# Optimization experiments

Hardware: AMD Instinct MI355X
Metric: run time of the kernel (lower is better)

## Reference

```python
import jax, jax.numpy as jnp
import numpy as np

B, HH, WW, C, HEADS = 2, 128, 128, 256, 8
D = C // HEADS


def setup_inputs() -> dict:
    key = jax.random.key(0)
    ks = jax.random.split(key, 24)
    def nrm(k, shape, s=0.02):
        return jax.random.normal(k, shape, jnp.float32) * s
    inp = {
        'x_2': jax.random.normal(ks[0], (B, HH, WW, C), jnp.float32),
        'x_4': jax.random.normal(ks[1], (B, HH, WW, C), jnp.float32),
        'x_8': jax.random.normal(ks[2], (B, HH, WW, C), jnp.float32),
        'y':   jax.random.normal(ks[3], (B, HH, WW, C), jnp.float32),
        'Wqm': nrm(ks[4], (C, C)), 'Wkm': nrm(ks[5], (C, C)), 'Wvm': nrm(ks[6], (C, C)),
        'Wk2': nrm(ks[7], (C, C)), 'Wv2': nrm(ks[8], (C, C)),
        'Wk4': nrm(ks[9], (C, C)), 'Wv4': nrm(ks[10], (C, C)),
        'Wk8': nrm(ks[11], (C, C)), 'Wv8': nrm(ks[12], (C, C)),
        'rescalem': jnp.ones((HEADS, 1, 1), jnp.float32),
        'rescale2': jnp.ones((HEADS, 1, 1), jnp.float32),
        'rescale4': jnp.ones((HEADS, 1, 1), jnp.float32),
        'rescale8': jnp.ones((HEADS, 1, 1), jnp.float32),
        'Wproj': nrm(ks[13], (C, C)), 'bproj': jnp.zeros((C,), jnp.float32),
        'Wpos1': nrm(ks[14], (C, 1, 3, 3)), 'Wpos2': nrm(ks[15], (C, 1, 3, 3)),
    }
    return inp


def _l2norm(x):
    # F.normalize(p=2, dim=-1): x / max(||x||_2, eps)
    return x / jnp.maximum(jnp.linalg.norm(x, axis=-1, keepdims=True), 1e-12)


def _heads_T(t):
    # (b, n, h*d) -> (b, h, d, n)  (split heads then transpose last two dims)
    b, n, _ = t.shape
    return t.reshape(b, n, HEADS, D).transpose(0, 2, 3, 1)


def _dwconv(x, w):
    # x: NCHW, w: (C,1,3,3) depthwise
    return jax.lax.conv_general_dilated(
        x, w, (1, 1), 'SAME',
        dimension_numbers=('NCHW', 'OIHW', 'NCHW'),
        feature_group_count=C)


def reference(x_2, x_4, x_8, y,
              Wqm, Wkm, Wvm, Wk2, Wv2, Wk4, Wv4, Wk8, Wv8,
              rescalem, rescale2, rescale4, rescale8,
              Wproj, bproj, Wpos1, Wpos2):
    b, h, w, c = y.shape
    n = h * w
    x2 = x_2.reshape(b, n, c)
    x4 = x_4.reshape(b, n, c)
    x8 = x_8.reshape(b, n, c)
    yf = y.reshape(b, n, c)

    q_inpm = yf @ Wqm.T
    v_inpm = yf @ Wvm.T
    qm = _l2norm(_heads_T(q_inpm))  # (b,heads,d,n), L2-normalized over n

    def branch(k_inp, v_inp, rescale):
        k = _l2norm(_heads_T(k_inp))   # (b,heads,d,n)
        v = _heads_T(v_inp)            # (b,heads,d,n)
        attn = jnp.einsum('bhdn,bhen->bhde', k, qm) * rescale  # (b,heads,d,d)
        attn = jax.nn.softmax(attn, axis=-1)
        return jnp.einsum('bhde,bhen->bhdn', attn, v)

    # NOTE: original code uses rescale4 for the x8 branch (faithful to source).
    xo = (branch(yf @ Wkm.T, v_inpm, rescalem)
          + branch(x2 @ Wk2.T, x2 @ Wv2.T, rescale2)
          + branch(x4 @ Wk4.T, x4 @ Wv4.T, rescale4)
          + branch(x8 @ Wk8.T, x8 @ Wv8.T, rescale4))

    # (b,heads,d,n) -> (b,n,heads*d)
    xo = xo.transpose(0, 3, 1, 2).reshape(b, n, HEADS * D)
    out_c = (xo @ Wproj.T + bproj).reshape(b, h, w, c)

    p = v_inpm.reshape(b, h, w, c).transpose(0, 3, 1, 2)  # NCHW
    p = _dwconv(p, Wpos1)
    p = jax.nn.gelu(p, approximate=False)
    p = _dwconv(p, Wpos2)
    out_p = p.transpose(0, 2, 3, 1)

    return out_c + out_p
```

## Files before the change

### kernel.cpp

```cpp
#include <hip/hip_runtime.h>
#include <hip/hip_bf16.h>
#include <math.h>

typedef short bf16x8 __attribute__((ext_vector_type(8)));
typedef float f32x4 __attribute__((ext_vector_type(4)));

#define MFMA16(a,b,c) __builtin_amdgcn_mfma_f32_16x16x32_bf16(a,b,c,0,0,0)

__device__ inline short f2bf(float f){
  union{ __hip_bfloat16 h; short s; } u;
  u.h = __float2bfloat16(f);
  return u.s;
}
__device__ inline float bf2f(short s){
  uint32_t u = ((uint32_t)(uint16_t)s) << 16;
  return __builtin_bit_cast(float, u);
}
__device__ inline void store8bf(short* dst, float4 a, float4 b){
  union{ short s[8]; int4 q; } u;
  u.s[0]=f2bf(a.x); u.s[1]=f2bf(a.y); u.s[2]=f2bf(a.z); u.s[3]=f2bf(a.w);
  u.s[4]=f2bf(b.x); u.s[5]=f2bf(b.y); u.s[6]=f2bf(b.z); u.s[7]=f2bf(b.w);
  *(int4*)dst = u.q;
}

__device__ inline void gld16(const void* g, void* l){
  __builtin_amdgcn_global_load_lds(
      (const __attribute__((address_space(1))) unsigned int*)g,
      (__attribute__((address_space(3))) unsigned int*)l, 16, 0, 0);
}

#define BARC() do{ asm volatile("":::"memory"); __builtin_amdgcn_s_barrier(); \
                   asm volatile("":::"memory"); }while(0)

__global__ __launch_bounds__(256) void k_cvt(const float* __restrict__ src, short* __restrict__ dst, int n){
  int i = blockIdx.x*256 + threadIdx.x;
  if(i < n) dst[i] = f2bf(src[i]);
}

__global__ __launch_bounds__(256) void k_wvt(const float* __restrict__ wm, const float* __restrict__ w2,
                                             const float* __restrict__ w4, const float* __restrict__ w8,
                                             short* __restrict__ wvT){
  int t = blockIdx.x*256 + threadIdx.x;
  int br = t >> 16; int rem = t & 65535; int a = rem >> 8, j = rem & 255;
  const float* w = (br==0)? wm : (br==1)? w2 : (br==2)? w4 : w8;
  wvT[t] = f2bf(w[j*256 + a]);
}

__global__ __launch_bounds__(256) void k_wT(const float* __restrict__ w1, const float* __restrict__ w2,
                                            float* __restrict__ wT){
  int t = blockIdx.x*256 + threadIdx.x;
  if(t >= 4608) return;
  int cv = t / 2304; int rem = t % 2304; int tap = rem >> 8; int c = rem & 255;
  const float* w = cv ? w2 : w1;
  wT[t] = w[c*9 + tap];
}

__global__ __launch_bounds__(256) void k_pack(const float* __restrict__ x2, const float* __restrict__ x4,
                                              const float* __restrict__ x8, const float* __restrict__ y,
                                              short* __restrict__ xt){
  int sb = blockIdx.z; int s = sb >> 1, b = sb & 1;
  const float* src = ((s==0)? y : (s==1)? x2 : (s==2)? x4 : x8) + (size_t)b*16384*256;
  __shared__ short tile[64*264];
  int t = threadIdx.x, l = t & 63, w = t >> 6;
  int n0 = blockIdx.x*64;
  #pragma unroll
  for(int p=0;p<16;++p){
    int row = p*4 + w;
    float4 v = *(const float4*)(src + (size_t)(n0+row)*256 + 4*l);
    union{ short s4[4]; int2 q; } u;
    u.s4[0]=f2bf(v.x); u.s4[1]=f2bf(v.y); u.s4[2]=f2bf(v.z); u.s4[3]=f2bf(v.w);
    *(int2*)&tile[row*264 + 4*l] = u.q;
  }
  __syncthreads();
  int c = t;
  short* outb = xt + ((size_t)sb*512 + (n0>>5))*8192;
  int sw = (c>>1)&3;
  #pragma unroll
  for(int ti=0; ti<2; ++ti){
    union{ short v[32]; int4 q4[4]; } rowv;
    #pragma unroll
    for(int j=0;j<32;++j) rowv.v[j] = tile[(ti*32+j)*264 + c];
    char* ob = (char*)(outb + (size_t)ti*8192 + c*32);
    #pragma unroll
    for(int hi=0;hi<4;++hi)
      *(int4*)(ob + ((hi ^ sw)<<4)) = rowv.q4[hi];
  }
}

__device__ inline bf16x8 tfrag(const short* base, int c, int hi){
  int byte = c*64 + ((hi ^ ((c>>1)&3))<<4);
  return *(const bf16x8*)((const char*)base + byte);
}

__global__ __launch_bounds__(512,2) void k_cov(const short* __restrict__ xt, float* __restrict__ covF){
  int jb = blockIdx.x;
  int ck = blockIdx.y;
  int j = jb >> 1, b = jb & 1;
  int t = threadIdx.x, l = t & 63, w = t >> 6;
  int lr = l & 15, hi = l >> 4;
  __shared__ short lds2[2][16384];
  int su = (j < 4) ? 0 : (j - 3);
  int sv = (j == 0) ? 0 : ((j < 4) ? j : (j - 3));
  int sym = (su == sv);
  const short* Ug = xt + (size_t)(su*2+b)*512*8192;
  const short* Vg = xt + (size_t)(sv*2+b)*512*8192;
  int nt0 = ck*32;

  f32x4 acc[2][16];
  #pragma unroll
  for(int i=0;i<2;++i)
    #pragma unroll
    for(int n2=0;n2<16;++n2) acc[i][n2] = (f32x4){0.f,0.f,0.f,0.f};

  #define STAGE_S(bufi, kk) do{                                                 \
    const short* Ut_ = Ug + (size_t)(nt0+(kk))*8192;                            \
    short* dst_ = &lds2[bufi][0];                                               \
    _Pragma("unroll")                                                           \
    for(int i_=0;i_<2;++i_){ int ch_ = w*2+i_;                                  \
      gld16(Ut_ + ch_*512 + l*8, dst_ + ch_*512); }                             \
  }while(0)
  #define STAGE_A(bufi, kk) do{                                                 \
    const short* Ut_ = Ug + (size_t)(nt0+(kk))*8192;                            \
    const short* Vt_ = Vg + (size_t)(nt0+(kk))*8192;                            \
    short* dst_ = &lds2[bufi][0];                                               \
    _Pragma("unroll")                                                           \
    for(int i_=0;i_<4;++i_){ int ch_ = w*4+i_;                                  \
      const short* g_ = (ch_<16) ? (Ut_ + ch_*512 + l*8)                        \
                                 : (Vt_ + (ch_-16)*512 + l*8);                  \
      gld16(g_, dst_ + ch_*512); }                                              \
  }while(0)

  #define COMPUTE(cur, vofs) do{                                                \
    const short* Ub_ = &lds2[cur][0];                                           \
    const short* Vb_ = Ub_ + (vofs);                                            \
    bf16x8 a0_ = tfrag(Ub_, w*32 + lr, hi);                                     \
    bf16x8 a1_ = tfrag(Ub_, w*32 + 16 + lr, hi);                                \
    _Pragma("unroll")                                                           \
    for(int nt_=0;nt_<16;++nt_){                                                \
      bf16x8 bb_ = tfrag(Vb_, nt_*16 + lr, hi);                                 \
      acc[0][nt_] = MFMA16(a0_, bb_, acc[0][nt_]);                              \
      acc[1][nt_] = MFMA16(a1_, bb_, acc[1][nt_]);                              \
    }                                                                           \
  }while(0)

  if(sym){
    STAGE_S(0, 0);
    STAGE_S(1, 1);
    asm volatile("s_waitcnt vmcnt(2)":::"memory");
    BARC();
    for(int k=0;k<32;++k){
      int cur = k & 1;
      COMPUTE(cur, 0);
      if(k == 31) break;
      BARC();
      if(k+2 < 32){
        STAGE_S(cur, k+2);
        asm volatile("s_waitcnt vmcnt(2)":::"memory");
      } else {
        asm volatile("s_waitcnt vmcnt(0)":::"memory");
      }
      BARC();
    }
  } else {
    STAGE_A(0, 0);
    STAGE_A(1, 1);
    asm volatile("s_waitcnt vmcnt(4)":::"memory");
    BARC();
    for(int k=0;k<32;++k){
      int cur = k & 1;
      COMPUTE(cur, 8192);
      if(k == 31) break;
      BARC();
      if(k+2 < 32){
        STAGE_A(cur, k+2);
        asm volatile("s_waitcnt vmcnt(4)":::"memory");
      } else {
        asm volatile("s_waitcnt vmcnt(0)":::"memory");
      }
      BARC();
    }
  }
  #undef STAGE_S
  #undef STAGE_A
  #undef COMPUTE

  float* cov = covF + (size_t)jb*65536;
  #pragma unroll
  for(int rt=0;rt<2;++rt)
    #pragma unroll
    for(int nt=0;nt<16;++nt)
      #pragma unroll
      for(int r=0;r<4;++r){
        int row = w*32 + rt*16 + 4*hi + r;
        int col = nt*16 + lr;
        atomicAdd(&cov[(size_t)row*256 + col], acc[rt][nt][r]);
      }
}

__device__ inline void mm_32x256(const short (*wA)[264], const short* __restrict__ covbf,
                                 short (*tmp)[264], int t){
  int l = t & 63, w = t >> 6;
  int mt = w >> 1, ntb = (w & 1)*8;
  f32x4 acc[8];
  #pragma unroll
  for(int i=0;i<8;++i) acc[i] = (f32x4){0.f,0.f,0.f,0.f};
  #pragma unroll
  for(int kk=0; kk<8; ++kk){
    bf16x8 a = *(const bf16x8*)&wA[16*mt + (l&15)][kk*32 + 8*(l>>4)];
    #pragma unroll
    for(int n=0; n<8; ++n){
      int j = (ntb+n)*16 + (l&15);
      bf16x8 bb = *(const bf16x8*)&covbf[(size_t)j*256 + kk*32 + 8*(l>>4)];
      acc[n] = MFMA16(a, bb, acc[n]);
    }
  }
  #pragma unroll
  for(int n=0;n<8;++n)
    #pragma unroll
    for(int r=0;r<4;++r)
      tmp[16*mt + 4*(l>>4) + r][(ntb+n)*16 + (l&15)] = f2bf(acc[n][r]);
}
__device__ inline void mm_32x32(const short (*A)[264], const short (*Bw)[264], float (*M)[33], int t){
  int l = t & 63, w = t >> 6;
  int mt = w >> 1, nt = w & 1;
  f32x4 acc = (f32x4){0.f,0.f,0.f,0.f};
  #pragma unroll
  for(int kk=0; kk<8; ++kk){
    bf16x8 a = *(const bf16x8*)&A[16*mt + (l&15)][kk*32 + 8*(l>>4)];
    bf16x8 b = *(const bf16x8*)&Bw[16*nt + (l&15)][kk*32 + 8*(l>>4)];
    acc = MFMA16(a, b, acc);
  }
  #pragma unroll
  for(int r=0;r<4;++r)
    M[16*mt + 4*(l>>4) + r][16*nt + (l&15)] = acc[r];
}

__global__ __launch_bounds__(256) void k_attn(
    const float* __restrict__ Wq, const float* __restrict__ Wkm, const float* __restrict__ Wk2,
    const float* __restrict__ Wk4, const float* __restrict__ Wk8,
    const float* __restrict__ rsm, const float* __restrict__ rs2, const float* __restrict__ rs4,
    const short* __restrict__ covB, float* __restrict__ Aout){
  int h = blockIdx.x, b = blockIdx.y, br = blockIdx.z;
  int t = threadIdx.x;
  __shared__ short wk[32][264], wq[32][264], tmp[32][264];
  __shared__ float Ml[32][33];
  __shared__ float nrm[64];
  const float* Wk = (br==0)? Wkm : (br==1)? Wk2 : (br==2)? Wk4 : Wk8;
  {
    int d = t >> 3, c0 = (t & 7)*32;
    const float* pk = Wk + (size_t)(h*32+d)*256 + c0;
    const float* pq = Wq + (size_t)(h*32+d)*256 + c0;
    #pragma unroll
    for(int i=0;i<32;i+=8){
      float4 a1 = *(const float4*)(pk+i), a2 = *(const float4*)(pk+i+4);
      store8bf(&wk[d][c0+i], a1, a2);
      float4 b1 = *(const float4*)(pq+i), b2 = *(const float4*)(pq+i+4);
      store8bf(&wq[d][c0+i], b1, b2);
    }
  }
  __syncthreads();
  const short* cxy = covB + (size_t)(br*2+b)*65536;
  const short* cxx = (br==0)? cxy : covB + (size_t)(8 + (br-1)*2 + b)*65536;
  const short* cyy = covB + (size_t)b*65536;
  mm_32x256(wk, cxx, tmp, t); __syncthreads();
  mm_32x32(tmp, wk, Ml, t);   __syncthreads();
  if(t < 32) nrm[t] = Ml[t][t];
  __syncthreads();
  mm_32x256(wq, cyy, tmp, t); __syncthreads();
  mm_32x32(tmp, wq, Ml, t);   __syncthreads();
  if(t < 32) nrm[32+t] = Ml[t][t];
  __syncthreads();
  mm_32x256(wk, cxy, tmp, t); __syncthreads();
  mm_32x32(tmp, wq, Ml, t);   __syncthreads();
  if(t < 32){
    int d = t;
    const float* rs = (br==0)? rsm : (br==1)? rs2 : rs4;
    float rsv = rs[h];
    float invk = 1.f / fmaxf(sqrtf(fmaxf(nrm[d], 0.f)), 1e-12f);
    float lg[32]; float mx = -1e30f;
    #pragma unroll
    for(int e=0;e<32;++e){
      float invq = 1.f / fmaxf(sqrtf(fmaxf(nrm[32+e], 0.f)), 1e-12f);
      float v = Ml[d][e] * invk * invq * rsv;
      lg[e] = v; mx = fmaxf(mx, v);
    }
    float sum = 0.f;
    #pragma unroll
    for(int e=0;e<32;++e){ lg[e] = expf(lg[e]-mx); sum += lg[e]; }
    float inv = 1.f/sum;
    float* Ao = Aout + ((size_t)((br*2+b)*8 + h))*1024 + d*32;
    #pragma unroll
    for(int e=0;e<32;++e) Ao[e] = lg[e]*inv;
  }
}

__global__ __launch_bounds__(256) void k_qfold(const float* __restrict__ Wproj, const float* __restrict__ Ain,
                                               const short* __restrict__ wvT, short* __restrict__ qf){
  int cg = blockIdx.x, b = blockIdx.y, br = blockIdx.z;
  int t = threadIdx.x;
  __shared__ float Al[8*1036];
  __shared__ short pl[32][264];
  const float* Ag = Ain + (size_t)((br*2+b)*8)*1024;
  for(int i=t; i<8192; i+=256){
    int hh = i >> 10, dd = (i >> 5) & 31, ee = i & 31;
    Al[hh*1036 + dd*32 + ee] = Ag[i];
  }
  __syncthreads();
  {
    int c = cg*32 + (t >> 3), h = t & 7;
    const float* wpr = Wproj + (size_t)c*256 + h*32;
    float wp[32];
    #pragma unroll
    for(int i=0;i<32;i+=4){
      float4 v = *(const float4*)(wpr+i);
      wp[i]=v.x; wp[i+1]=v.y; wp[i+2]=v.z; wp[i+3]=v.w;
    }
    float pv[32];
    #pragma unroll
    for(int e=0;e<32;++e) pv[e]=0.f;
    const float* Ah = Al + h*1036;
    #pragma unroll
    for(int d=0; d<32; ++d){
      float wpd = wp[d];
      #pragma unroll
      for(int e=0;e<32;e+=4){
        float4 av = *(const float4*)&Ah[d*32+e];
        pv[e]   += wpd*av.x; pv[e+1] += wpd*av.y;
        pv[e+2] += wpd*av.z; pv[e+3] += wpd*av.w;
      }
    }
    #pragma unroll
    for(int e=0;e<32;++e) pl[t>>3][h*32+e] = f2bf(pv[e]);
  }
  __syncthreads();
  {
    int l = t & 63, w = t >> 6, mt = w >> 1, ntb = (w & 1)*8;
    const short* wvt = wvT + (size_t)br*65536;
    f32x4 acc[8];
    #pragma unroll
    for(int i=0;i<8;++i) acc[i] = (f32x4){0.f,0.f,0.f,0.f};
    #pragma unroll
    for(int kk=0; kk<8; ++kk){
      bf16x8 a = *(const bf16x8*)&pl[16*mt + (l&15)][kk*32 + 8*(l>>4)];
      #pragma unroll
      for(int n=0;n<8;++n){
        int arow = (ntb+n)*16 + (l&15);
        bf16x8 bb = *(const bf16x8*)&wvt[(size_t)arow*256 + kk*32 + 8*(l>>4)];
        acc[n] = MFMA16(a, bb, acc[n]);
      }
    }
    short* qfp = qf + (size_t)(br*2+b)*65536;
    #pragma unroll
    for(int n=0;n<8;++n)
      #pragma unroll
      for(int r=0;r<4;++r){
        int row = cg*32 + 16*mt + 4*(l>>4) + r;
        int col = (ntb+n)*16 + (l&15);
        qfp[(size_t)row*256 + col] = f2bf(acc[n][r]);
      }
  }
}

__device__ inline void at_write4(short* base, int row, int l, float4 v){
  union{ short s[4]; int2 q; } u;
  u.s[0]=f2bf(v.x); u.s[1]=f2bf(v.y); u.s[2]=f2bf(v.z); u.s[3]=f2bf(v.w);
  int byte = row*512 + 8*l;
  byte ^= ((row&7)<<4);
  *(int2*)((char*)base + byte) = u.q;
}
__device__ inline bf16x8 at_read8(const short* base, int row, int kk, int q){
  int byte = row*512 + kk*64 + q*16;
  byte ^= ((row&7)<<4);
  return *(const bf16x8*)((const char*)base + byte);
}

__global__ __launch_bounds__(256,2) void k_vm(const float* __restrict__ y, const short* __restrict__ wB,
                                              short* __restrict__ vm){
  int t = threadIdx.x, l = t & 63, w = t >> 6;
  size_t m0 = (size_t)blockIdx.x*64;
  __shared__ short at[64*256];
  #pragma unroll
  for(int rr=0; rr<16; ++rr){
    int row = w*16 + rr;
    float4 v = *(const float4*)(y + (m0+row)*256 + 4*l);
    at_write4(at, row, l, v);
  }
  __syncthreads();
  f32x4 acc[4][4];
  #pragma unroll
  for(int i=0;i<4;++i)
    #pragma unroll
    for(int n2=0;n2<4;++n2) acc[i][n2] = (f32x4){0.f,0.f,0.f,0.f};
  #pragma unroll
  for(int kk=0; kk<8; ++kk){
    bf16x8 a[4];
    #pragma unroll
    for(int rt=0;rt<4;++rt) a[rt] = at_read8(at, rt*16 + (l&15), kk, l>>4);
    #pragma unroll
    for(int nt=0;nt<4;++nt){
      int bc = (w*4+nt)*16 + (l&15);
      bf16x8 bb = *(const bf16x8*)&wB[(size_t)bc*256 + kk*32 + 8*(l>>4)];
      #pragma unroll
      for(int rt=0;rt<4;++rt) acc[rt][nt] = MFMA16(a[rt], bb, acc[rt][nt]);
    }
  }
  #pragma unroll
  for(int rt=0;rt<4;++rt)
    #pragma unroll
    for(int nt=0;nt<4;++nt)
      #pragma unroll
      for(int r=0;r<4;++r){
        size_t row = m0 + rt*16 + 4*(l>>4) + r;
        int col = (w*4+nt)*16 + (l&15);
        vm[row*256 + col] = f2bf(acc[rt][nt][r]);
      }
}

__global__ __launch_bounds__(256) void k_conv(const short* __restrict__ in, const float* __restrict__ wT,
                                              short* __restrict__ out, int do_gelu){
  int tid = blockIdx.x*256 + threadIdx.x;
  int cg = tid & 31; int pix = tid >> 5;
  int x = pix & 127, yy = (pix >> 7) & 127, b = pix >> 14;
  int c0 = cg*8;
  float acc[8];
  #pragma unroll
  for(int i=0;i<8;++i) acc[i]=0.f;
  #pragma unroll
  for(int ky=0; ky<3; ++ky){
    int sy = yy + ky - 1;
    if(sy < 0 || sy > 127) continue;
    #pragma unroll
    for(int kx=0; kx<3; ++kx){
      int sx = x + kx - 1;
      if(sx < 0 || sx > 127) continue;
      const float* wp = wT + (ky*3+kx)*256 + c0;
      float4 w0 = *(const float4*)wp;
      float4 w1 = *(const float4*)(wp+4);
      const short* p = in + ((size_t)(((b<<7)+sy)<<7) + sx)*256 + c0;
      union{ int4 q; short s[8]; } u;
      u.q = *(const int4*)p;
      acc[0] += bf2f(u.s[0])*w0.x; acc[1] += bf2f(u.s[1])*w0.y;
      acc[2] += bf2f(u.s[2])*w0.z; acc[3] += bf2f(u.s[3])*w0.w;
      acc[4] += bf2f(u.s[4])*w1.x; acc[5] += bf2f(u.s[5])*w1.y;
      acc[6] += bf2f(u.s[6])*w1.z; acc[7] += bf2f(u.s[7])*w1.w;
    }
  }
  if(do_gelu){
    #pragma unroll
    for(int cc=0;cc<8;++cc)
      acc[cc] = 0.5f*acc[cc]*(1.f + erff(acc[cc]*0.70710678118654752f));
  }
  union{ int4 q; short s[8]; } o;
  #pragma unroll
  for(int cc=0;cc<8;++cc) o.s[cc] = f2bf(acc[cc]);
  *(int4*)(out + (size_t)pix*256 + c0) = o.q;
}

__global__ __launch_bounds__(256,2) void k_final(const float* __restrict__ y, const float* __restrict__ x2,
                                                 const float* __restrict__ x4, const float* __restrict__ x8,
                                                 const short* __restrict__ qf, const float* __restrict__ bproj,
                                                 const short* __restrict__ pos, float* __restrict__ out){
  int t = threadIdx.x, l = t & 63, w = t >> 6;
  size_t m0 = (size_t)blockIdx.x*64;
  int b = (int)(m0 >> 14);
  __shared__ short at[64*256];
  f32x4 acc[4][4];
  #pragma unroll
  for(int i=0;i<4;++i)
    #pragma unroll
    for(int n2=0;n2<4;++n2) acc[i][n2] = (f32x4){0.f,0.f,0.f,0.f};
  const float* srcs[4] = {y, x2, x4, x8};
  #pragma unroll 1
  for(int br=0; br<4; ++br){
    __syncthreads();
    #pragma unroll
    for(int rr=0; rr<16; ++rr){
      int row = w*16 + rr;
      float4 v = *(const float4*)(srcs[br] + (m0+row)*256 + 4*l);
      at_write4(at, row, l, v);
    }
    __syncthreads();
    const short* qb = qf + (size_t)(br*2+b)*65536;
    #pragma unroll
    for(int kk=0; kk<8; ++kk){
      bf16x8 a[4];
      #pragma unroll
      for(int rt=0;rt<4;++rt) a[rt] = at_read8(at, rt*16 + (l&15), kk, l>>4);
      #pragma unroll
      for(int nt=0;nt<4;++nt){
        int bc = (w*4+nt)*16 + (l&15);
        bf16x8 bb = *(const bf16x8*)&qb[(size_t)bc*256 + kk*32 + 8*(l>>4)];
        #pragma unroll
        for(int rt=0;rt<4;++rt) acc[rt][nt] = MFMA16(a[rt], bb, acc[rt][nt]);
      }
    }
  }
  #pragma unroll
  for(int rt=0;rt<4;++rt)
    #pragma unroll
    for(int nt=0;nt<4;++nt)
      #pragma unroll
      for(int r=0;r<4;++r){
        size_t row = m0 + rt*16 + 4*(l>>4) + r;
        int col = (w*4+nt)*16 + (l&15);
        out[row*256 + col] = acc[rt][nt][r] + bproj[col] + bf2f(pos[row*256 + col]);
      }
}

extern "C" void kernel_launch(void* const* d_in, const int* in_sizes, int n_in,
                              void* d_out, int out_size, void* d_ws, size_t ws_size,
                              hipStream_t stream){
  (void)in_sizes; (void)n_in; (void)out_size; (void)ws_size;
  const float* x2   = (const float*)d_in[0];
  const float* x4   = (const float*)d_in[1];
  const float* x8   = (const float*)d_in[2];
  const float* y    = (const float*)d_in[3];
  const float* Wq   = (const float*)d_in[4];
  const float* Wkm  = (const float*)d_in[5];
  const float* Wvm  = (const float*)d_in[6];
  const float* Wk2  = (const float*)d_in[7];
  const float* Wv2  = (const float*)d_in[8];
  const float* Wk4  = (const float*)d_in[9];
  const float* Wv4  = (const float*)d_in[10];
  const float* Wk8  = (const float*)d_in[11];
  const float* Wv8  = (const float*)d_in[12];
  const float* rsm  = (const float*)d_in[13];
  const float* rs2  = (const float*)d_in[14];
  const float* rs4  = (const float*)d_in[15];
  const float* Wproj= (const float*)d_in[17];
  const float* bproj= (const float*)d_in[18];
  const float* Wp1  = (const float*)d_in[19];
  const float* Wp2  = (const float*)d_in[20];
  float* out = (float*)d_out;

  char* ws = (char*)d_ws;
  short* XT2  = (short*)(ws + 0);
  short* VM   = (short*)(ws + 0);
  short* GBUF = (short*)(ws + 16777216);
  short* POS  = (short*)(ws + 33554432);
  float* wT   = (float*)(ws + 50331648);
  float* covF = (float*)(ws + 67108864);
  short* covB = (short*)(ws + 70778880);
  float* Aout = (float*)(ws + 72613888);
  short* QF   = (short*)(ws + 72876032);
  short* WvmB = (short*)(ws + 73924608);
  short* WvT  = (short*)(ws + 74055680);

  hipMemsetAsync(covF, 0, 3670016, stream);
  k_cvt  <<<256, 256, 0, stream>>>(Wvm, WvmB, 65536);
  k_wvt  <<<1024, 256, 0, stream>>>(Wvm, Wv2, Wv4, Wv8, WvT);
  k_pack <<<dim3(256,1,8), 256, 0, stream>>>(x2, x4, x8, y, XT2);
  k_cov  <<<dim3(14,16), 512, 0, stream>>>(XT2, covF);
  k_cvt  <<<3584, 256, 0, stream>>>(covF, covB, 917504);
  k_wT   <<<18, 256, 0, stream>>>(Wp1, Wp2, wT);
  k_attn <<<dim3(8,2,4), 256, 0, stream>>>(Wq, Wkm, Wk2, Wk4, Wk8, rsm, rs2, rs4, covB, Aout);
  k_qfold<<<dim3(8,2,4), 256, 0, stream>>>(Wproj, Aout, WvT, QF);
  k_vm   <<<512, 256, 0, stream>>>(y, WvmB, VM);
  k_conv <<<4096, 256, 0, stream>>>(VM, wT, GBUF, 1);
  k_conv <<<4096, 256, 0, stream>>>(GBUF, wT + 2304, POS, 0);
  k_final<<<512, 256, 0, stream>>>(y, x2, x4, x8, QF, bproj, POS, out);
}
```

Measured before the change: 288.2 us.

## Reuse bf16 row-major inputs, triple-buffer covariance, split atomic accumulation copies

k_pack now also writes a row-major bf16 copy of all four inputs. The V projection and final kernels read that copy instead of re-reading and converting the fp32 inputs. The covariance kernel moves from double to triple LDS buffering and spreads its accumulation across four copies indexed by chunk, which a new conversion kernel sums. This path runs only when the workspace is large enough, and it costs extra workspace, more LDS per block, and a larger memset.

```diff
diff --git a/kernel.cpp b/kernel.cpp
--- a/kernel.cpp
+++ b/kernel.cpp
@@ -35,6 +35,15 @@
 __global__ __launch_bounds__(256) void k_cvt(const float* __restrict__ src, short* __restrict__ dst, int n){
   int i = blockIdx.x*256 + threadIdx.x;
   if(i < n) dst[i] = f2bf(src[i]);
+}
+
+__global__ __launch_bounds__(256) void k_cvtN(const float* __restrict__ src, short* __restrict__ dst,
+                                              int n, int ncpy){
+  int i = blockIdx.x*256 + threadIdx.x;
+  if(i >= n) return;
+  float s = src[i];
+  for(int c=1;c<ncpy;++c) s += src[i + (size_t)c*917504];
+  dst[i] = f2bf(s);
 }
 
 __global__ __launch_bounds__(256) void k_wvt(const float* __restrict__ wm, const float* __restrict__ w2,
@@ -57,7 +66,7 @@
 
 __global__ __launch_bounds__(256) void k_pack(const float* __restrict__ x2, const float* __restrict__ x4,
                                               const float* __restrict__ x8, const float* __restrict__ y,
-                                              short* __restrict__ xt){
+                                              short* __restrict__ xt, short* __restrict__ xb){
   int sb = blockIdx.z; int s = sb >> 1, b = sb & 1;
   const float* src = ((s==0)? y : (s==1)? x2 : (s==2)? x4 : x8) + (size_t)b*16384*256;
   __shared__ short tile[64*264];
@@ -70,6 +79,7 @@
     union{ short s4[4]; int2 q; } u;
     u.s4[0]=f2bf(v.x); u.s4[1]=f2bf(v.y); u.s4[2]=f2bf(v.z); u.s4[3]=f2bf(v.w);
     *(int2*)&tile[row*264 + 4*l] = u.q;
+    if(xb) *(int2*)(xb + ((size_t)sb*16384 + n0 + row)*256 + 4*l) = u.q;
   }
   __syncthreads();
   int c = t;
@@ -92,13 +102,14 @@
   return *(const bf16x8*)((const char*)base + byte);
 }
 
-__global__ __launch_bounds__(512,2) void k_cov(const short* __restrict__ xt, float* __restrict__ covF){
+__global__ __launch_bounds__(512,2) void k_cov(const short* __restrict__ xt, float* __restrict__ covF,
+                                               int ncpy){
   int jb = blockIdx.x;
   int ck = blockIdx.y;
   int j = jb >> 1, b = jb & 1;
   int t = threadIdx.x, l = t & 63, w = t >> 6;
   int lr = l & 15, hi = l >> 4;
-  __shared__ short lds2[2][16384];
+  __shared__ short lds3[3][16384];
   int su = (j < 4) ? 0 : (j - 3);
   int sv = (j == 0) ? 0 : ((j < 4) ? j : (j - 3));
   int sym = (su == sv);
@@ -114,7 +125,7 @@
 
   #define STAGE_S(bufi, kk) do{                                                 \
     const short* Ut_ = Ug + (size_t)(nt0+(kk))*8192;                            \
-    short* dst_ = &lds2[bufi][0];                                               \
+    short* dst_ = &lds3[bufi][0];                                               \
     _Pragma("unroll")                                                           \
     for(int i_=0;i_<2;++i_){ int ch_ = w*2+i_;                                  \
       gld16(Ut_ + ch_*512 + l*8, dst_ + ch_*512); }                             \
@@ -122,16 +133,15 @@
   #define STAGE_A(bufi, kk) do{                                                 \
     const short* Ut_ = Ug + (size_t)(nt0+(kk))*8192;                            \
     const short* Vt_ = Vg + (size_t)(nt0+(kk))*8192;                            \
-    short* dst_ = &lds2[bufi][0];                                               \
+    short* dst_ = &lds3[bufi][0];                                               \
     _Pragma("unroll")                                                           \
     for(int i_=0;i_<4;++i_){ int ch_ = w*4+i_;                                  \
       const short* g_ = (ch_<16) ? (Ut_ + ch_*512 + l*8)                        \
                                  : (Vt_ + (ch_-16)*512 + l*8);                  \
       gld16(g_, dst_ + ch_*512); }                                              \
   }while(0)
-
-  #define COMPUTE(cur, vofs) do{                                                \
-    const short* Ub_ = &lds2[cur][0];                                           \
+  #define COMPUTE(bufp, vofs) do{                                               \
+    const short* Ub_ = bufp;                                                    \
     const short* Vb_ = Ub_ + (vofs);                                            \
     bf16x8 a0_ = tfrag(Ub_, w*32 + lr, hi);                                     \
     bf16x8 a1_ = tfrag(Ub_, w*32 + 16 + lr, hi);                                \
@@ -144,47 +154,53 @@
   }while(0)
 
   if(sym){
-    STAGE_S(0, 0);
-    STAGE_S(1, 1);
-    asm volatile("s_waitcnt vmcnt(2)":::"memory");
+    STAGE_S(0,0); STAGE_S(1,1); STAGE_S(2,2);
+    asm volatile("s_waitcnt vmcnt(4)":::"memory");
     BARC();
+    int buf = 0;
+    #pragma unroll 1
     for(int k=0;k<32;++k){
-      int cur = k & 1;
-      COMPUTE(cur, 0);
-      if(k == 31) break;
+      COMPUTE(&lds3[buf][0], 0);
+      if(k==31) break;
       BARC();
-      if(k+2 < 32){
-        STAGE_S(cur, k+2);
+      if(k < 29){
+        STAGE_S(buf, k+3);
+        asm volatile("s_waitcnt vmcnt(4)":::"memory");
+      } else if(k == 29){
         asm volatile("s_waitcnt vmcnt(2)":::"memory");
       } else {
         asm volatile("s_waitcnt vmcnt(0)":::"memory");
       }
       BARC();
+      buf = (buf==2)?0:(buf+1);
     }
   } else {
-    STAGE_A(0, 0);
-    STAGE_A(1, 1);
-    asm volatile("s_waitcnt vmcnt(4)":::"memory");
+    STAGE_A(0,0); STAGE_A(1,1); STAGE_A(2,2);
+    asm volatile("s_waitcnt vmcnt(8)":::"memory");
     BARC();
+    int buf = 0;
+    #pragma unroll 1
     for(int k=0;k<32;++k){
-      int cur = k & 1;
-      COMPUTE(cur, 8192);
-      if(k == 31) break;
+      COMPUTE(&lds3[buf][0], 8192);
+      if(k==31) break;
       BARC();
-      if(k+2 < 32){
-        STAGE_A(cur, k+2);
+      if(k < 29){
+        STAGE_A(buf, k+3);
+        asm volatile("s_waitcnt vmcnt(8)":::"memory");
+      } else if(k == 29){
         asm volatile("s_waitcnt vmcnt(4)":::"memory");
       } else {
         asm volatile("s_waitcnt vmcnt(0)":::"memory");
       }
       BARC();
+      buf = (buf==2)?0:(buf+1);
     }
   }
   #undef STAGE_S
   #undef STAGE_A
   #undef COMPUTE
 
-  float* cov = covF + (size_t)jb*65536;
+  float* cov = covF + (size_t)(ck & (ncpy-1))*917504 + (size_t)jb*65536;
   #pragma unroll
   for(int rt=0;rt<2;++rt)
     #pragma unroll
@@ -416,6 +432,42 @@
       }
 }
 
+__global__ __launch_bounds__(256) void k_vm_g(const short* __restrict__ xb, const short* __restrict__ wB,
+                                              short* __restrict__ vm){
+  int t = threadIdx.x, l = t & 63, w = t >> 6;
+  size_t m0 = (size_t)blockIdx.x*64;
+  int lr = l & 15, hq = (l >> 4)*8;
+  f32x4 acc[4][4];
+  #pragma unroll
+  for(int i=0;i<4;++i)
+    #pragma unroll
+    for(int n2=0;n2<4;++n2) acc[i][n2] = (f32x4){0.f,0.f,0.f,0.f};
+  #pragma unroll
+  for(int kk=0; kk<8; ++kk){
+    int k = kk*32 + hq;
+    bf16x8 a[4];
+    #pragma unroll
+    for(int rt=0;rt<4;++rt)
+      a[rt] = *(const bf16x8*)(xb + (m0 + rt*16 + lr)*256 + k);
+    #pragma unroll
+    for(int nt=0;nt<4;++nt){
+      bf16x8 bb = *(const bf16x8*)(wB + (size_t)((w*4+nt)*16 + lr)*256 + k);
+      #pragma unroll
+      for(int rt=0;rt<4;++rt) acc[rt][nt] = MFMA16(a[rt], bb, acc[rt][nt]);
+    }
+  }
+  #pragma unroll
+  for(int rt=0;rt<4;++rt)
+    #pragma unroll
+    for(int nt=0;nt<4;++nt)
+      #pragma unroll
+      for(int r=0;r<4;++r){
+        size_t row = m0 + rt*16 + 4*(l>>4) + r;
+        int col = (w*4+nt)*16 + lr;
+        vm[row*256 + col] = f2bf(acc[rt][nt][r]);
+      }
+}
+
 __global__ __launch_bounds__(256) void k_conv(const short* __restrict__ in, const float* __restrict__ wT,
                                               short* __restrict__ out, int do_gelu){
   int tid = blockIdx.x*256 + threadIdx.x;
@@ -507,10 +559,53 @@
       }
 }
 
+__global__ __launch_bounds__(256) void k_final_g(const short* __restrict__ xb, const short* __restrict__ qf,
+                                                 const float* __restrict__ bproj, const short* __restrict__ pos,
+                                                 float* __restrict__ out){
+  int t = threadIdx.x, l = t & 63, w = t >> 6;
+  size_t m0 = (size_t)blockIdx.x*64;
+  int b = (int)(m0 >> 14);
+  int lr = l & 15, hq = (l >> 4)*8;
+  f32x4 acc[4][4];
+  #pragma unroll
+  for(int i=0;i<4;++i)
+    #pragma unroll
+    for(int n2=0;n2<4;++n2) acc[i][n2] = (f32x4){0.f,0.f,0.f,0.f};
+  #pragma unroll 1
+  for(int br=0; br<4; ++br){
+    const short* src = xb + (size_t)br*2*16384*256;
+    const short* qb = qf + (size_t)(br*2+b)*65536;
+    #pragma unroll
+    for(int kk=0; kk<8; ++kk){
+      int k = kk*32 + hq;
+      bf16x8 a[4];
+      #pragma unroll
+      for(int rt=0;rt<4;++rt)
+        a[rt] = *(const bf16x8*)(src + (m0 + rt*16 + lr)*256 + k);
+      #pragma unroll
+      for(int nt=0;nt<4;++nt){
+        bf16x8 bb = *(const bf16x8*)(qb + (size_t)((w*4+nt)*16 + lr)*256 + k);
+        #pragma unroll
+        for(int rt=0;rt<4;++rt) acc[rt][nt] = MFMA16(a[rt], bb, acc[rt][nt]);
+      }
+    }
+  }
+  #pragma unroll
+  for(int rt=0;rt<4;++rt)
+    #pragma unroll
+    for(int nt=0;nt<4;++nt)
+      #pragma unroll
+      for(int r=0;r<4;++r){
+        size_t row = m0 + rt*16 + 4*(l>>4) + r;
+        int col = (w*4+nt)*16 + lr;
+        out[row*256 + col] = acc[rt][nt][r] + bproj[col] + bf2f(pos[row*256 + col]);
+      }
+}
+
 extern "C" void kernel_launch(void* const* d_in, const int* in_sizes, int n_in,
                               void* d_out, int out_size, void* d_ws, size_t ws_size,
                               hipStream_t stream){
-  (void)in_sizes; (void)n_in; (void)out_size; (void)ws_size;
+  (void)in_sizes; (void)n_in; (void)out_size;
   const float* x2   = (const float*)d_in[0];
   const float* x4   = (const float*)d_in[1];
   const float* x8   = (const float*)d_in[2];
@@ -539,24 +634,45 @@
   short* GBUF = (short*)(ws + 16777216);
   short* POS  = (short*)(ws + 33554432);
   float* wT   = (float*)(ws + 50331648);
-  float* covF = (float*)(ws + 67108864);
-  short* covB = (short*)(ws + 70778880);
-  float* Aout = (float*)(ws + 72613888);
-  short* QF   = (short*)(ws + 72876032);
-  short* WvmB = (short*)(ws + 73924608);
-  short* WvT  = (short*)(ws + 74055680);
-
-  hipMemsetAsync(covF, 0, 3670016, stream);
+
+  const size_t NEED_BIG = 152698880;
+  bool big = (ws_size >= NEED_BIG);
+
+  short* XB; float* covF; short* covB; float* Aout; short* QF; short* WvmB; short* WvT;
+  int ncpy;
+  if(big){
+    XB   = (short*)(ws + 67108864);
+    covF = (float*)(ws + 134217728);
+    covB = (short*)(ws + 148897792);
+    Aout = (float*)(ws + 150732800);
+    QF   = (short*)(ws + 150994944);
+    WvmB = (short*)(ws + 152043520);
+    WvT  = (short*)(ws + 152174592);
+    ncpy = 4;
+  } else {
+    XB   = nullptr;
+    covF = (float*)(ws + 67108864);
+    covB = (short*)(ws + 70778880);
+    Aout = (float*)(ws + 72613888);
+    QF   = (short*)(ws + 72876032);
+    WvmB = (short*)(ws + 73924608);
+    WvT  = (short*)(ws + 74055680);
+    ncpy = 1;
+  }
+
+  hipMemsetAsync(covF, 0, (size_t)ncpy*3670016, stream);
   k_cvt  <<<256, 256, 0, stream>>>(Wvm, WvmB, 65536);
   k_wvt  <<<1024, 256, 0, stream>>>(Wvm, Wv2, Wv4, Wv8, WvT);
-  k_pack <<<dim3(256,1,8), 256, 0, stream>>>(x2, x4, x8, y, XT2);
-  k_cov  <<<dim3(14,16), 512, 0, stream>>>(XT2, covF);
-  k_cvt  <<<3584, 256, 0, stream>>>(covF, covB, 917504);
+  k_pack <<<dim3(256,1,8), 256, 0, stream>>>(x2, x4, x8, y, XT2, XB);
+  k_cov  <<<dim3(14,16), 512, 0, stream>>>(XT2, covF, ncpy);
+  k_cvtN <<<3584, 256, 0, stream>>>(covF, covB, 917504, ncpy);
   k_wT   <<<18, 256, 0, stream>>>(Wp1, Wp2, wT);
   k_attn <<<dim3(8,2,4), 256, 0, stream>>>(Wq, Wkm, Wk2, Wk4, Wk8, rsm, rs2, rs4, covB, Aout);
   k_qfold<<<dim3(8,2,4), 256, 0, stream>>>(Wproj, Aout, WvT, QF);
-  k_vm   <<<512, 256, 0, stream>>>(y, WvmB, VM);
+  if(big) k_vm_g<<<512, 256, 0, stream>>>(XB, WvmB, VM);
+  else    k_vm  <<<512, 256, 0, stream>>>(y, WvmB, VM);
   k_conv <<<4096, 256, 0, stream>>>(VM, wT, GBUF, 1);
   k_conv <<<4096, 256, 0, stream>>>(GBUF, wT + 2304, POS, 0);
-  k_final<<<512, 256, 0, stream>>>(y, x2, x4, x8, QF, bproj, POS, out);
-}
+  if(big) k_final_g<<<512, 256, 0, stream>>>(XB, QF, bproj, POS, out);
+  else    k_final  <<<512, 256, 0, stream>>>(y, x2, x4, x8, QF, bproj, POS, out);
+}
```

Result: slower. 321.1 us (+11.4%).

## Triple-buffer covariance k_cov loads and replace atomics with per-chunk partial sums

Applied to the files above, without the earlier changes.

The covariance kernel moves from double to triple buffering in LDS, so loads run three K-steps ahead, and the loop is no longer unrolled. When the workspace is large enough, each K-chunk block writes its partial covariance to its own slice instead of atomically adding into a shared buffer. A new conversion kernel then sums the 16 partials while converting to bf16, which also removes the memset. This cuts atomic contention and exposed load latency, at the cost of more LDS per block (possible occupancy loss) and extra global traffic for the partial buffers.

```diff
diff --git a/kernel.cpp b/kernel.cpp
--- a/kernel.cpp
+++ b/kernel.cpp
@@ -35,6 +35,15 @@
 __global__ __launch_bounds__(256) void k_cvt(const float* __restrict__ src, short* __restrict__ dst, int n){
   int i = blockIdx.x*256 + threadIdx.x;
   if(i < n) dst[i] = f2bf(src[i]);
+}
+
+__global__ __launch_bounds__(256) void k_cvtN(const float* __restrict__ src, short* __restrict__ dst,
+                                              int n, int ncpy){
+  int i = blockIdx.x*256 + threadIdx.x;
+  if(i >= n) return;
+  float s = src[i];
+  for(int c=1;c<ncpy;++c) s += src[i + (size_t)c*917504];
+  dst[i] = f2bf(s);
 }
 
 __global__ __launch_bounds__(256) void k_wvt(const float* __restrict__ wm, const float* __restrict__ w2,
@@ -92,13 +101,14 @@
   return *(const bf16x8*)((const char*)base + byte);
 }
 
-__global__ __launch_bounds__(512,2) void k_cov(const short* __restrict__ xt, float* __restrict__ covF){
+__global__ __launch_bounds__(512,2) void k_cov(const short* __restrict__ xt, float* __restrict__ covF,
+                                               int plain){
   int jb = blockIdx.x;
   int ck = blockIdx.y;
   int j = jb >> 1, b = jb & 1;
   int t = threadIdx.x, l = t & 63, w = t >> 6;
   int lr = l & 15, hi = l >> 4;
-  __shared__ short lds2[2][16384];
+  __shared__ short lds3[3][16384];
   int su = (j < 4) ? 0 : (j - 3);
   int sv = (j == 0) ? 0 : ((j < 4) ? j : (j - 3));
   int sym = (su == sv);
@@ -114,7 +124,7 @@
 
   #define STAGE_S(bufi, kk) do{                                                 \
     const short* Ut_ = Ug + (size_t)(nt0+(kk))*8192;                            \
-    short* dst_ = &lds2[bufi][0];                                               \
+    short* dst_ = &lds3[bufi][0];                                               \
     _Pragma("unroll")                                                           \
     for(int i_=0;i_<2;++i_){ int ch_ = w*2+i_;                                  \
       gld16(Ut_ + ch_*512 + l*8, dst_ + ch_*512); }                             \
@@ -122,16 +132,15 @@
   #define STAGE_A(bufi, kk) do{                                                 \
     const short* Ut_ = Ug + (size_t)(nt0+(kk))*8192;                            \
     const short* Vt_ = Vg + (size_t)(nt0+(kk))*8192;                            \
-    short* dst_ = &lds2[bufi][0];                                               \
+    short* dst_ = &lds3[bufi][0];                                               \
     _Pragma("unroll")                                                           \
     for(int i_=0;i_<4;++i_){ int ch_ = w*4+i_;                                  \
       const short* g_ = (ch_<16) ? (Ut_ + ch_*512 + l*8)                        \
                                  : (Vt_ + (ch_-16)*512 + l*8);                  \
       gld16(g_, dst_ + ch_*512); }                                              \
   }while(0)
-
-  #define COMPUTE(cur, vofs) do{                                                \
-    const short* Ub_ = &lds2[cur][0];                                           \
+  #define COMPUTE(bufp, vofs) do{                                               \
+    const short* Ub_ = bufp;                                                    \
     const short* Vb_ = Ub_ + (vofs);                                            \
     bf16x8 a0_ = tfrag(Ub_, w*32 + lr, hi);                                     \
     bf16x8 a1_ = tfrag(Ub_, w*32 + 16 + lr, hi);                                \
@@ -144,57 +153,77 @@
   }while(0)
 
   if(sym){
-    STAGE_S(0, 0);
-    STAGE_S(1, 1);
-    asm volatile("s_waitcnt vmcnt(2)":::"memory");
+    STAGE_S(0,0); STAGE_S(1,1); STAGE_S(2,2);
+    asm volatile("s_waitcnt vmcnt(4)":::"memory");
     BARC();
+    int buf = 0;
+    #pragma unroll 1
     for(int k=0;k<32;++k){
-      int cur = k & 1;
-      COMPUTE(cur, 0);
-      if(k == 31) break;
+      COMPUTE(&lds3[buf][0], 0);
+      if(k==31) break;
       BARC();
-      if(k+2 < 32){
-        STAGE_S(cur, k+2);
+      if(k < 29){
+        STAGE_S(buf, k+3);
+        asm volatile("s_waitcnt vmcnt(4)":::"memory");
+      } else if(k == 29){
         asm volatile("s_waitcnt vmcnt(2)":::"memory");
       } else {
         asm volatile("s_waitcnt vmcnt(0)":::"memory");
       }
       BARC();
+      buf = (buf==2)?0:(buf+1);
     }
   } else {
-    STAGE_A(0, 0);
-    STAGE_A(1, 1);
-    asm volatile("s_waitcnt vmcnt(4)":::"memory");
+    STAGE_A(0,0); STAGE_A(1,1); STAGE_A(2,2);
+    asm volatile("s_waitcnt vmcnt(8)":::"memory");
     BARC();
+    int buf = 0;
+    #pragma unroll 1
     for(int k=0;k<32;++k){
-      int cur = k & 1;
-      COMPUTE(cur, 8192);
-      if(k == 31) break;
+      COMPUTE(&lds3[buf][0], 8192);
+      if(k==31) break;
       BARC();
-      if(k+2 < 32){
-        STAGE_A(cur, k+2);
+      if(k < 29){
+        STAGE_A(buf, k+3);
+        asm volatile("s_waitcnt vmcnt(8)":::"memory");
+      } else if(k == 29){
         asm volatile("s_waitcnt vmcnt(4)":::"memory");
       } else {
         asm volatile("s_waitcnt vmcnt(0)":::"memory");
       }
       BARC();
+      buf = (buf==2)?0:(buf+1);
     }
   }
   #undef STAGE_S
   #undef STAGE_A
   #undef COMPUTE
 
-  float* cov = covF + (size_t)jb*65536;
-  #pragma unroll
-  for(int rt=0;rt<2;++rt)
-    #pragma unroll
-    for(int nt=0;nt<16;++nt)
-      #pragma unroll
-      for(int r=0;r<4;++r){
-        int row = w*32 + rt*16 + 4*hi + r;
-        int col = nt*16 + lr;
-        atomicAdd(&cov[(size_t)row*256 + col], acc[rt][nt][r]);
-      }
+  if(plain){
+    float* cov = covF + (size_t)ck*917504 + (size_t)jb*65536;
+    #pragma unroll
+    for(int rt=0;rt<2;++rt)
+      #pragma unroll
+      for(int nt=0;nt<16;++nt)
+        #pragma unroll
+        for(int r=0;r<4;++r){
+          int row = w*32 + rt*16 + 4*hi + r;
+          int col = nt*16 + lr;
+          cov[(size_t)row*256 + col] = acc[rt][nt][r];
+        }
+  } else {
+    float* cov = covF + (size_t)jb*65536;
+    #pragma unroll
+    for(int rt=0;rt<2;++rt)
+      #pragma unroll
+      for(int nt=0;nt<16;++nt)
+        #pragma unroll
+        for(int r=0;r<4;++r){
+          int row = w*32 + rt*16 + 4*hi + r;
+          int col = nt*16 + lr;
+          atomicAdd(&cov[(size_t)row*256 + col], acc[rt][nt][r]);
+        }
+  }
 }
 
 __device__ inline void mm_32x256(const short (*wA)[264], const short* __restrict__ covbf,
@@ -510,7 +539,7 @@
 extern "C" void kernel_launch(void* const* d_in, const int* in_sizes, int n_in,
                               void* d_out, int out_size, void* d_ws, size_t ws_size,
                               hipStream_t stream){
-  (void)in_sizes; (void)n_in; (void)out_size; (void)ws_size;
+  (void)in_sizes; (void)n_in; (void)out_size;
   const float* x2   = (const float*)d_in[0];
   const float* x4   = (const float*)d_in[1];
   const float* x8   = (const float*)d_in[2];
@@ -539,19 +568,33 @@
   short* GBUF = (short*)(ws + 16777216);
   short* POS  = (short*)(ws + 33554432);
   float* wT   = (float*)(ws + 50331648);
-  float* covF = (float*)(ws + 67108864);
-  short* covB = (short*)(ws + 70778880);
-  float* Aout = (float*)(ws + 72613888);
-  short* QF   = (short*)(ws + 72876032);
-  short* WvmB = (short*)(ws + 73924608);
-  short* WvT  = (short*)(ws + 74055680);
-
-  hipMemsetAsync(covF, 0, 3670016, stream);
+
+  const size_t NEED16 = 129630208;
+  int plain = (ws_size >= NEED16) ? 1 : 0;
+
+  float* covF; short* covB; float* Aout; short* QF; short* WvmB; short* WvT;
+  if(plain){
+    covF = (float*)(ws + 67108864);
+    covB = (short*)(ws + 125829120);
+    Aout = (float*)(ws + 127664128);
+    QF   = (short*)(ws + 127926272);
+    WvmB = (short*)(ws + 128974848);
+    WvT  = (short*)(ws + 129105920);
+  } else {
+    covF = (float*)(ws + 67108864);
+    covB = (short*)(ws + 70778880);
+    Aout = (float*)(ws + 72613888);
+    QF   = (short*)(ws + 72876032);
+    WvmB = (short*)(ws + 73924608);
+    WvT  = (short*)(ws + 74055680);
+  }
+
+  if(!plain) hipMemsetAsync(covF, 0, 3670016, stream);
   k_cvt  <<<256, 256, 0, stream>>>(Wvm, WvmB, 65536);
   k_wvt  <<<1024, 256, 0, stream>>>(Wvm, Wv2, Wv4, Wv8, WvT);
   k_pack <<<dim3(256,1,8), 256, 0, stream>>>(x2, x4, x8, y, XT2);
-  k_cov  <<<dim3(14,16), 512, 0, stream>>>(XT2, covF);
-  k_cvt  <<<3584, 256, 0, stream>>>(covF, covB, 917504);
+  k_cov  <<<dim3(14,16), 512, 0, stream>>>(XT2, covF, plain);
+  k_cvtN <<<3584, 256, 0, stream>>>(covF, covB, 917504, plain ? 16 : 1);
   k_wT   <<<18, 256, 0, stream>>>(Wp1, Wp2, wT);
   k_attn <<<dim3(8,2,4), 256, 0, stream>>>(Wq, Wkm, Wk2, Wk4, Wk8, rsm, rs2, rs4, covB, Aout);
   k_qfold<<<dim3(8,2,4), 256, 0, stream>>>(Wproj, Aout, WvT, QF);
```

Measured after the change: 261.9 us. 9.1% less time.
